# Kernel tuning notes

Hardware: AMD Instinct MI355X
Metric: run time of the kernel (lower is better)

## Reference

```python
import jax, jax.numpy as jnp
import numpy as np

# Problem sizes
N, D, B = 4096, 2048, 64  # nodes, feature dim, sequential samples
# LARFDSSOM hyperparameters (from __init__ defaults)
A_T = 0.3          # activation threshold
DSBETA = 1e-4      # moving-average rate
E_B = 0.5          # winner learning rate
E_N = 0.01 * E_B   # neighbor learning rate (e_n is multiplied by e_b in __init__)
EPS_DS = 0.01      # relevance smoothing


def setup_inputs() -> dict:
    key = jax.random.key(0)
    k0, k1, k2, k3, k4 = jax.random.split(key, 5)
    return {
        "x": jax.random.uniform(k0, (B, D), jnp.float32),
        "weights": jax.random.uniform(k1, (N, D), jnp.float32),
        "moving_avg": jax.random.uniform(k2, (N, D), jnp.float32),
        "relevances": jax.random.uniform(k3, (N, D), jnp.float32),
        "wins": jnp.zeros((N,), jnp.float32),
        "neighbors": jax.random.randint(k4, (N, N), 0, 2) > 0,
    }


def _som_steps(x, weights, moving_avg, relevances, wins, neighbors):
    """Sequential LARFDSSOM update_map over B samples (codebook at max size,
    so the add_node branch is structurally impossible and the per-sample step
    is either 'update winner + neighbors' or a no-op)."""
    node_ids = jnp.arange(weights.shape[0])

    def step(state, w):
        W, M, R, wn = state
        diff = w[None, :] - W                          # [N, D]
        # weighted_distance + activation
        dists = jnp.sum(R * diff * diff, axis=1)       # [N]
        rel_sum = jnp.sum(R, axis=1)                   # [N]
        act = rel_sum / (rel_sum + dists + 1e-7)
        winner = jnp.argmax(act)
        do_upd = act[winner] >= A_T                    # else no-op (codebook full)
        is_winner = node_ids == winner
        is_nb = neighbors[winner] & (~is_winner)
        # per-node learning rate: e_b for winner, e_n for neighbors, 0 otherwise
        lr = jnp.where(is_winner, E_B, jnp.where(is_nb, E_N, 0.0))[:, None]  # [N, 1]
        # update_node (vectorized over all nodes, masked below)
        dist_abs = jnp.abs(diff)
        M_new = lr * DSBETA * dist_abs + (1.0 - lr * DSBETA) * M
        mx = jnp.max(M_new, axis=1, keepdims=True)
        mn = jnp.min(M_new, axis=1, keepdims=True)
        av = jnp.mean(M_new, axis=1, keepdims=True)
        denom = EPS_DS * (mx - mn)
        # denom == 0 -> original produces NaN then sets relevance to 1.0
        arg = jnp.clip((M_new - av) / jnp.where(denom == 0.0, 1.0, denom), -80.0, 80.0)
        R_new = jnp.where(denom == 0.0, 1.0, 1.0 / (1.0 + jnp.exp(arg)))
        W_new = W + lr * diff
        m = (do_upd & (lr[:, 0] > 0.0))[:, None]       # rows actually touched
        W = jnp.where(m, W_new, W)
        M = jnp.where(m, M_new, M)
        R = jnp.where(m, R_new, R)
        wn = wn + jnp.where(is_winner & do_upd, 1.0, 0.0)
        return (W, M, R, wn), None

    (W, M, R, wn), _ = jax.lax.scan(step, (weights, moving_avg, relevances, wins), x)
    return W


def reference(x, weights, moving_avg, relevances, wins, neighbors):
    return _som_steps(x, weights, moving_avg, relevances, wins, neighbors)
```

## Files before the change

### kernel.cpp

```cpp
#include <hip/hip_runtime.h>
#include <cstddef>

#define NN 4096
#define DD 2048
#define BB 64
#define RPB 8
#define NBLK (NN / RPB)

constexpr float kAT     = 0.3f;
constexpr float kDSBETA = 1e-4f;
constexpr float kEB     = 0.5f;
constexpr float kEN     = 0.005f;
constexpr float kEPS    = 0.01f;

__device__ __forceinline__ float wave_sum_f(float v) {
#pragma unroll
    for (int o = 32; o; o >>= 1) v += __shfl_xor(v, o, 64);
    return v;
}
__device__ __forceinline__ double wave_sum_d(double v) {
#pragma unroll
    for (int o = 32; o; o >>= 1) v += __shfl_xor(v, o, 64);
    return v;
}
__device__ __forceinline__ float wave_max_f(float v) {
#pragma unroll
    for (int o = 32; o; o >>= 1) v = fmaxf(v, __shfl_xor(v, o, 64));
    return v;
}
__device__ __forceinline__ float wave_min_f(float v) {
#pragma unroll
    for (int o = 32; o; o >>= 1) v = fminf(v, __shfl_xor(v, o, 64));
    return v;
}
__device__ __forceinline__ unsigned long long wave_max_u64(unsigned long long v) {
#pragma unroll
    for (int o = 32; o; o >>= 1) {
        const unsigned long long u = __shfl_xor(v, o, 64);
        v = (u > v) ? u : v;
    }
    return v;
}

__global__ void detect_nb(const unsigned char* __restrict__ nb, unsigned* __restrict__ flag) {
    unsigned v = 0;
    const int i0 = threadIdx.x * 256;
    for (int i = 0; i < 256; i++) {
        const int idx = i0 + i;
        if ((idx & 3) != 0) v |= nb[idx];
    }
    if (v != 0) atomicOr(flag, 1u);
}

__global__ __launch_bounds__(256, 2) void som_persist(
    const float* __restrict__ x,
    const float* __restrict__ W0,
    const float* __restrict__ M0,
    const float* __restrict__ R0,
    const unsigned char* __restrict__ nbb,
    const unsigned* __restrict__ flag,
    float* __restrict__ Wout,
    unsigned long long* __restrict__ pkey,
    unsigned long long* __restrict__ bcast)
{
    const int tid  = threadIdx.x;
    const int wid  = tid >> 6;
    const int lane = tid & 63;
    const int bid  = (int)blockIdx.x;
    const int n0   = bid * RPB;
    const int col  = tid * 8;

    __shared__ double sdd[2][RPB][4];
    __shared__ float  sf[3][4];
    __shared__ unsigned long long skk[RPB];
    __shared__ unsigned long long sKey;

    const bool nb_byte = (*flag != 0);
    const int* nbi = (const int*)nbb;

    float w[RPB][8], r[RPB][8], m[RPB][8], xcur[8];

#pragma unroll
    for (int row = 0; row < RPB; ++row) {
        const size_t base = (size_t)(n0 + row) * DD + col;
        *(float4*)(&w[row][0]) = *(const float4*)(W0 + base);
        *(float4*)(&w[row][4]) = *(const float4*)(W0 + base + 4);
        *(float4*)(&r[row][0]) = *(const float4*)(R0 + base);
        *(float4*)(&r[row][4]) = *(const float4*)(R0 + base + 4);
        *(float4*)(&m[row][0]) = *(const float4*)(M0 + base);
        *(float4*)(&m[row][4]) = *(const float4*)(M0 + base + 4);
    }
    *(float4*)(xcur)     = *(const float4*)(x + col);
    *(float4*)(xcur + 4) = *(const float4*)(x + col + 4);

    auto act_phase = [&](int slot) {
#pragma unroll
        for (int row = 0; row < RPB; ++row) {
            double pd = 0.0, ps = 0.0;
#pragma unroll
            for (int j = 0; j < 8; ++j) {
                const double d  = (double)xcur[j] - (double)w[row][j];
                const double rj = (double)r[row][j];
                pd += rj * d * d;
                ps += rj;
            }
            pd = wave_sum_d(pd); ps = wave_sum_d(ps);
            if (lane == 0) { sdd[0][row][wid] = pd; sdd[1][row][wid] = ps; }
        }
        __syncthreads();
        if (tid < RPB) {
            const int row = tid;
            const double td = sdd[0][row][0] + sdd[0][row][1] + sdd[0][row][2] + sdd[0][row][3];
            const double tr = sdd[1][row][0] + sdd[1][row][1] + sdd[1][row][2] + sdd[1][row][3];
            const double act = tr / (tr + td + 1e-7);
            const unsigned long long ab = (unsigned long long)__double_as_longlong(act);
            skk[row] = (ab & ~0xFFFULL) | (unsigned long long)(4095 - (n0 + row));
        }
        __syncthreads();
        if (tid == 0) {
            unsigned long long k = skk[0];
#pragma unroll
            for (int i = 1; i < RPB; ++i) k = (skk[i] > k) ? skk[i] : k;
            __hip_atomic_store(&pkey[(size_t)slot * NBLK + bid], k,
                               __ATOMIC_RELAXED, __HIP_MEMORY_SCOPE_AGENT);
        }
        __syncthreads();
    };

    act_phase(0);

    for (int t = 0; t < BB; ++t) {
        if (wid == 0) {
            unsigned long long kmax = 0;
            if (bid == 0) {
                unsigned long long* pk = pkey + (size_t)t * NBLK;
                unsigned long long kk[8];
                int it = 0;
                while (true) {
                    bool miss = false;
#pragma unroll
                    for (int i = 0; i < 8; ++i) {
                        kk[i] = __hip_atomic_load(&pk[lane + 64 * i],
                                                  __ATOMIC_RELAXED, __HIP_MEMORY_SCOPE_AGENT);
                        miss |= (kk[i] == 0ull);
                    }
                    if (!__any(miss)) break;
                    if (++it > 2000000) break;
                    __builtin_amdgcn_s_sleep(1);
                }
#pragma unroll
                for (int i = 0; i < 8; ++i) kmax = (kk[i] > kmax) ? kk[i] : kmax;
                kmax = wave_max_u64(kmax);
                if (lane < 8)
                    __hip_atomic_store(&bcast[((size_t)t * 8 + lane) * 8], kmax,
                                       __ATOMIC_RELAXED, __HIP_MEMORY_SCOPE_AGENT);
            } else {
                const int rep = bid & 7;
                int it = 0;
                while ((kmax = __hip_atomic_load(&bcast[((size_t)t * 8 + rep) * 8],
                                                 __ATOMIC_RELAXED, __HIP_MEMORY_SCOPE_AGENT))
                       == 0ull) {
                    if (++it > 2000000) break;
                    __builtin_amdgcn_s_sleep(4);
                }
            }
            if (lane == 0) sKey = kmax;
        }
        __syncthreads();
        const unsigned long long k = sKey;
        __syncthreads();
        const double act_w = __longlong_as_double((long long)(k & ~0xFFFULL));
        const int winner   = 4095 - (int)(k & 0xFFFULL);

        if (act_w >= (double)kAT) {
#pragma unroll
            for (int row = 0; row < RPB; ++row) {
                const int n = n0 + row;
                float lr = 0.0f;
                if (n == winner) {
                    lr = kEB;
                } else {
                    const size_t off = (size_t)winner * NN + n;
                    const bool isnb = nb_byte ? (nbb[off] != 0) : (nbi[off] != 0);
                    if (isnb) lr = kEN;
                }
                if (lr != 0.0f) {
                    const float c1 = lr * kDSBETA;
                    const float c2 = 1.0f - c1;
                    float psum = 0.0f, pmx = -INFINITY, pmn = INFINITY;
#pragma unroll
                    for (int j = 0; j < 8; ++j) {
                        const float d  = xcur[j] - w[row][j];
                        const float mv = c1 * fabsf(d) + c2 * m[row][j];
                        w[row][j] += lr * d;
                        m[row][j] = mv;
                        psum += mv;
                        pmx = fmaxf(pmx, mv);
                        pmn = fminf(pmn, mv);
                    }
                    psum = wave_sum_f(psum); pmx = wave_max_f(pmx); pmn = wave_min_f(pmn);
                    if (lane == 0) { sf[0][wid] = psum; sf[1][wid] = pmx; sf[2][wid] = pmn; }
                    __syncthreads();
                    const float ts  = sf[0][0] + sf[0][1] + sf[0][2] + sf[0][3];
                    const float tmx = fmaxf(fmaxf(sf[1][0], sf[1][1]), fmaxf(sf[1][2], sf[1][3]));
                    const float tmn = fminf(fminf(sf[2][0], sf[2][1]), fminf(sf[2][2], sf[2][3]));
                    __syncthreads();
                    const float av    = ts * (1.0f / (float)DD);
                    const float denom = kEPS * (tmx - tmn);
                    if (denom == 0.0f) {
#pragma unroll
                        for (int j = 0; j < 8; ++j) r[row][j] = 1.0f;
                    } else {
#pragma unroll
                        for (int j = 0; j < 8; ++j) {
                            float a = (m[row][j] - av) / denom;
                            a = fminf(fmaxf(a, -80.0f), 80.0f);
                            r[row][j] = 1.0f / (1.0f + expf(a));
                        }
                    }
                }
            }
        }

        if (t < BB - 1) {
            const size_t xb = (size_t)(t + 1) * DD + col;
            *(float4*)(xcur)     = *(const float4*)(x + xb);
            *(float4*)(xcur + 4) = *(const float4*)(x + xb + 4);
            act_phase(t + 1);
        }
    }

#pragma unroll
    for (int row = 0; row < RPB; ++row) {
        const size_t base = (size_t)(n0 + row) * DD + col;
        *(float4*)(Wout + base)     = *(float4*)(&w[row][0]);
        *(float4*)(Wout + base + 4) = *(float4*)(&w[row][4]);
    }
}

__global__ __launch_bounds__(256) void som_step(
    const float* __restrict__ x_upd, const float* __restrict__ x_act,
    float* __restrict__ W, float* __restrict__ M, float* __restrict__ R,
    const void* __restrict__ nb, const unsigned* __restrict__ flag,
    const unsigned long long* __restrict__ part_upd,
    unsigned long long* __restrict__ part_act)
{
    const int n   = blockIdx.x;
    const int tid = threadIdx.x;
    __shared__ float  sred[3][4];
    __shared__ double sredd[2][4];

    float lr = 0.0f;
    if (part_upd != nullptr) {
        unsigned long long k = part_upd[(size_t)(tid & 63) * 8];
        k = wave_max_u64(k);
        const double act_w = __longlong_as_double((long long)(k & ~0xFFFULL));
        const int winner   = 4095 - (int)(k & 0xFFFULL);
        if (act_w >= (double)kAT) {
            if (n == winner) lr = kEB;
            else {
                const size_t off = (size_t)winner * NN + n;
                const bool isnb = (*flag != 0)
                    ? (((const unsigned char*)nb)[off] != 0)
                    : (((const int*)nb)[off] != 0);
                if (isnb) lr = kEN;
            }
        }
    }
    const bool next = (x_act != nullptr);
    if (lr == 0.0f && !next) return;

    const size_t rowoff = (size_t)n * DD + (size_t)tid * 8;
    const size_t xoff   = (size_t)tid * 8;
    float w[8], r[8];
    *(float4*)(w)     = *(const float4*)(W + rowoff);
    *(float4*)(w + 4) = *(const float4*)(W + rowoff + 4);

    if (lr != 0.0f) {
        float m[8], xu[8], mnew[8];
        *(float4*)(m)      = *(const float4*)(M + rowoff);
        *(float4*)(m + 4)  = *(const float4*)(M + rowoff + 4);
        *(float4*)(xu)     = *(const float4*)(x_upd + xoff);
        *(float4*)(xu + 4) = *(const float4*)(x_upd + xoff + 4);
        const float c1 = lr * kDSBETA, c2 = 1.0f - c1;
        float psum = 0.0f, pmx = -INFINITY, pmn = INFINITY;
#pragma unroll
        for (int j = 0; j < 8; j++) {
            const float d = xu[j] - w[j];
            w[j] += lr * d;
            const float mv = c1 * fabsf(d) + c2 * m[j];
            mnew[j] = mv; psum += mv;
            pmx = fmaxf(pmx, mv); pmn = fminf(pmn, mv);
        }
        psum = wave_sum_f(psum); pmx = wave_max_f(pmx); pmn = wave_min_f(pmn);
        const int wid = tid >> 6, lane = tid & 63;
        if (lane == 0) { sred[0][wid] = psum; sred[1][wid] = pmx; sred[2][wid] = pmn; }
        __syncthreads();
        const float ts  = sred[0][0] + sred[0][1] + sred[0][2] + sred[0][3];
        const float tmx = fmaxf(fmaxf(sred[1][0], sred[1][1]), fmaxf(sred[1][2], sred[1][3]));
        const float tmn = fminf(fminf(sred[2][0], sred[2][1]), fminf(sred[2][2], sred[2][3]));
        __syncthreads();
        const float av = ts * (1.0f / (float)DD);
        const float denom = kEPS * (tmx - tmn);
        if (denom == 0.0f) {
#pragma unroll
            for (int j = 0; j < 8; j++) r[j] = 1.0f;
        } else {
#pragma unroll
            for (int j = 0; j < 8; j++) {
                float a = (mnew[j] - av) / denom;
                a = fminf(fmaxf(a, -80.0f), 80.0f);
                r[j] = 1.0f / (1.0f + expf(a));
            }
        }
        *(float4*)(W + rowoff)     = *(float4*)(w);
        *(float4*)(W + rowoff + 4) = *(float4*)(w + 4);
        *(float4*)(M + rowoff)     = *(float4*)(mnew);
        *(float4*)(M + rowoff + 4) = *(float4*)(mnew + 4);
        *(float4*)(R + rowoff)     = *(float4*)(r);
        *(float4*)(R + rowoff + 4) = *(float4*)(r + 4);
    } else {
        *(float4*)(r)     = *(const float4*)(R + rowoff);
        *(float4*)(r + 4) = *(const float4*)(R + rowoff + 4);
    }

    if (next) {
        float xn[8];
        *(float4*)(xn)     = *(const float4*)(x_act + xoff);
        *(float4*)(xn + 4) = *(const float4*)(x_act + xoff + 4);
        double pd = 0.0, ps = 0.0;
#pragma unroll
        for (int j = 0; j < 8; j++) {
            const double d  = (double)xn[j] - (double)w[j];
            const double rj = (double)r[j];
            pd += rj * d * d; ps += rj;
        }
        pd = wave_sum_d(pd); ps = wave_sum_d(ps);
        const int wid = tid >> 6, lane = tid & 63;
        if (lane == 0) { sredd[0][wid] = pd; sredd[1][wid] = ps; }
        __syncthreads();
        if (tid == 0) {
            const double td = sredd[0][0] + sredd[0][1] + sredd[0][2] + sredd[0][3];
            const double tr = sredd[1][0] + sredd[1][1] + sredd[1][2] + sredd[1][3];
            const double act = tr / (tr + td + 1e-7);
            const unsigned long long ab = (unsigned long long)__double_as_longlong(act);
            const unsigned long long kk = (ab & ~0xFFFULL) | (unsigned long long)(4095 - n);
            atomicMax(&part_act[(size_t)(n & 63) * 8], kk);
        }
    }
}

extern "C" void kernel_launch(void* const* d_in, const int* in_sizes, int n_in,
                              void* d_out, int out_size, void* d_ws, size_t ws_size,
                              hipStream_t stream) {
    const float*         x   = (const float*)d_in[0];
    const float*         W0  = (const float*)d_in[1];
    float*               M   = (float*)d_in[2];
    float*               R   = (float*)d_in[3];
    const unsigned char* nbb = (const unsigned char*)d_in[5];
    float*               W   = (float*)d_out;

    unsigned long long* part = (unsigned long long*)d_ws;
    const size_t part_bytes  = (size_t)66 * 64 * 8 * sizeof(unsigned long long);
    unsigned long long* bcast = (unsigned long long*)((char*)d_ws + part_bytes);
    const size_t cnt_bytes = (size_t)BB * 8 * 16 * sizeof(unsigned);
    unsigned* flagp = (unsigned*)((char*)d_ws + part_bytes + cnt_bytes);

    hipMemsetAsync(d_ws, 0, part_bytes + cnt_bytes + 64, stream);
    detect_nb<<<1, 256, 0, stream>>>(nbb, flagp);

    int occ = 0;
    hipError_t qerr = hipOccupancyMaxActiveBlocksPerMultiprocessor(
        &occ, (const void*)som_persist, 256, 0);
    if (qerr == hipSuccess && occ >= 2) {
        som_persist<<<NBLK, 256, 0, stream>>>(x, W0, M, R, nbb, flagp, W, part, bcast);
        return;
    }

    hipMemcpyAsync(W, W0, sizeof(float) * (size_t)NN * DD, hipMemcpyDeviceToDevice, stream);
    som_step<<<NN, 256, 0, stream>>>(nullptr, x, W, M, R, nbb, flagp, nullptr, part);
    for (int t = 0; t < BB; t++) {
        const float* xu = x + (size_t)t * DD;
        const float* xa = (t < BB - 1) ? (x + (size_t)(t + 1) * DD) : nullptr;
        const unsigned long long* pu = part + (size_t)t * 64 * 8;
        unsigned long long*       pa = (t < BB - 1) ? (part + (size_t)(t + 1) * 64 * 8) : nullptr;
        som_step<<<NN, 256, 0, stream>>>(xu, xa, W, M, R, nbb, flagp, pu, pa);
    }
}
```

Baseline: 1.686 ms.

## Decentralize winner reduction and batch per-row block reductions in persistent SOM kernel

Every block now polls all 512 partial keys and reduces the winner itself, replacing the two-hop path through block 0 and a broadcast slot. The per-row shared-memory reductions are batched behind one barrier instead of two barriers per updated row. The neighbor flags are read with one vector load, and the next sample's x is prefetched early. Several redundant __syncthreads are removed. In exchange, all 512 blocks poll the same key array, which adds L2 traffic and contention.

New measurement: 1.681 ms (median of 2 runs). About the same (-0.3%).

```diff
diff --git a/kernel.cpp b/kernel.cpp
--- a/kernel.cpp
+++ b/kernel.cpp
@@ -60,8 +60,7 @@
     const unsigned char* __restrict__ nbb,
     const unsigned* __restrict__ flag,
     float* __restrict__ Wout,
-    unsigned long long* __restrict__ pkey,
-    unsigned long long* __restrict__ bcast)
+    unsigned long long* __restrict__ pkey)
 {
     const int tid  = threadIdx.x;
     const int wid  = tid >> 6;
@@ -71,7 +70,7 @@
     const int col  = tid * 8;
 
     __shared__ double sdd[2][RPB][4];
-    __shared__ float  sf[3][4];
+    __shared__ float  sf[3][RPB][4];
     __shared__ unsigned long long skk[RPB];
     __shared__ unsigned long long sKey;
 
@@ -124,67 +123,73 @@
             __hip_atomic_store(&pkey[(size_t)slot * NBLK + bid], k,
                                __ATOMIC_RELAXED, __HIP_MEMORY_SCOPE_AGENT);
         }
-        __syncthreads();
     };
 
     act_phase(0);
 
+    float xn[8];
     for (int t = 0; t < BB; ++t) {
+        const bool has_next = (t < BB - 1);
+        if (has_next) {
+            const size_t xb = (size_t)(t + 1) * DD + col;
+            *(float4*)(xn)     = *(const float4*)(x + xb);
+            *(float4*)(xn + 4) = *(const float4*)(x + xb + 4);
+        }
+
         if (wid == 0) {
+            unsigned long long* pk = pkey + (size_t)t * NBLK;
+            unsigned long long kk[8];
+            int it = 0;
+            while (true) {
+                bool miss = false;
+#pragma unroll
+                for (int i = 0; i < 8; ++i) {
+                    kk[i] = __hip_atomic_load(&pk[lane + 64 * i],
+                                              __ATOMIC_RELAXED, __HIP_MEMORY_SCOPE_AGENT);
+                    miss |= (kk[i] == 0ull);
+                }
+                if (!__any(miss)) break;
+                if (++it > 2000000) break;
+                __builtin_amdgcn_s_sleep(1);
+            }
             unsigned long long kmax = 0;
-            if (bid == 0) {
-                unsigned long long* pk = pkey + (size_t)t * NBLK;
-                unsigned long long kk[8];
-                int it = 0;
-                while (true) {
-                    bool miss = false;
-#pragma unroll
-                    for (int i = 0; i < 8; ++i) {
-                        kk[i] = __hip_atomic_load(&pk[lane + 64 * i],
-                                                  __ATOMIC_RELAXED, __HIP_MEMORY_SCOPE_AGENT);
-                        miss |= (kk[i] == 0ull);
-                    }
-                    if (!__any(miss)) break;
-                    if (++it > 2000000) break;
-                    __builtin_amdgcn_s_sleep(1);
-                }
-#pragma unroll
-                for (int i = 0; i < 8; ++i) kmax = (kk[i] > kmax) ? kk[i] : kmax;
-                kmax = wave_max_u64(kmax);
-                if (lane < 8)
-                    __hip_atomic_store(&bcast[((size_t)t * 8 + lane) * 8], kmax,
-                                       __ATOMIC_RELAXED, __HIP_MEMORY_SCOPE_AGENT);
-            } else {
-                const int rep = bid & 7;
-                int it = 0;
-                while ((kmax = __hip_atomic_load(&bcast[((size_t)t * 8 + rep) * 8],
-                                                 __ATOMIC_RELAXED, __HIP_MEMORY_SCOPE_AGENT))
-                       == 0ull) {
-                    if (++it > 2000000) break;
-                    __builtin_amdgcn_s_sleep(4);
-                }
-            }
+#pragma unroll
+            for (int i = 0; i < 8; ++i) kmax = (kk[i] > kmax) ? kk[i] : kmax;
+            kmax = wave_max_u64(kmax);
             if (lane == 0) sKey = kmax;
         }
         __syncthreads();
         const unsigned long long k = sKey;
-        __syncthreads();
         const double act_w = __longlong_as_double((long long)(k & ~0xFFFULL));
         const int winner   = 4095 - (int)(k & 0xFFFULL);
 
         if (act_w >= (double)kAT) {
+            int nbr[RPB];
+            {
+                const size_t off = (size_t)winner * NN + n0;
+                if (nb_byte) {
+                    const unsigned long long nb8 = *(const unsigned long long*)(nbb + off);
+#pragma unroll
+                    for (int i = 0; i < RPB; ++i)
+                        nbr[i] = (int)((nb8 >> (8 * i)) & 0xFFull);
+                } else {
+                    const int4 a = *(const int4*)(nbi + off);
+                    const int4 b = *(const int4*)(nbi + off + 4);
+                    nbr[0] = a.x; nbr[1] = a.y; nbr[2] = a.z; nbr[3] = a.w;
+                    nbr[4] = b.x; nbr[5] = b.y; nbr[6] = b.z; nbr[7] = b.w;
+                }
+            }
+            float lrs[RPB];
+            bool any = false;
 #pragma unroll
             for (int row = 0; row < RPB; ++row) {
                 const int n = n0 + row;
                 float lr = 0.0f;
-                if (n == winner) {
-                    lr = kEB;
-                } else {
-                    const size_t off = (size_t)winner * NN + n;
-                    const bool isnb = nb_byte ? (nbb[off] != 0) : (nbi[off] != 0);
-                    if (isnb) lr = kEN;
-                }
+                if (n == winner)      lr = kEB;
+                else if (nbr[row])    lr = kEN;
+                lrs[row] = lr;
                 if (lr != 0.0f) {
+                    any = true;
                     const float c1 = lr * kDSBETA;
                     const float c2 = 1.0f - c1;
                     float psum = 0.0f, pmx = -INFINITY, pmn = INFINITY;
@@ -199,33 +204,40 @@
                         pmn = fminf(pmn, mv);
                     }
                     psum = wave_sum_f(psum); pmx = wave_max_f(pmx); pmn = wave_min_f(pmn);
-                    if (lane == 0) { sf[0][wid] = psum; sf[1][wid] = pmx; sf[2][wid] = pmn; }
-                    __syncthreads();
-                    const float ts  = sf[0][0] + sf[0][1] + sf[0][2] + sf[0][3];
-                    const float tmx = fmaxf(fmaxf(sf[1][0], sf[1][1]), fmaxf(sf[1][2], sf[1][3]));
-                    const float tmn = fminf(fminf(sf[2][0], sf[2][1]), fminf(sf[2][2], sf[2][3]));
-                    __syncthreads();
-                    const float av    = ts * (1.0f / (float)DD);
-                    const float denom = kEPS * (tmx - tmn);
-                    if (denom == 0.0f) {
-#pragma unroll
-                        for (int j = 0; j < 8; ++j) r[row][j] = 1.0f;
-                    } else {
-#pragma unroll
-                        for (int j = 0; j < 8; ++j) {
-                            float a = (m[row][j] - av) / denom;
-                            a = fminf(fmaxf(a, -80.0f), 80.0f);
-                            r[row][j] = 1.0f / (1.0f + expf(a));
+                    if (lane == 0) { sf[0][row][wid] = psum; sf[1][row][wid] = pmx; sf[2][row][wid] = pmn; }
+                }
+            }
+            if (any) {
+                __syncthreads();
+#pragma unroll
+                for (int row = 0; row < RPB; ++row) {
+                    if (lrs[row] != 0.0f) {
+                        const float ts  = sf[0][row][0] + sf[0][row][1] + sf[0][row][2] + sf[0][row][3];
+                        const float tmx = fmaxf(fmaxf(sf[1][row][0], sf[1][row][1]),
+                                                fmaxf(sf[1][row][2], sf[1][row][3]));
+                        const float tmn = fminf(fminf(sf[2][row][0], sf[2][row][1]),
+                                                fminf(sf[2][row][2], sf[2][row][3]));
+                        const float av    = ts * (1.0f / (float)DD);
+                        const float denom = kEPS * (tmx - tmn);
+                        if (denom == 0.0f) {
+#pragma unroll
+                            for (int j = 0; j < 8; ++j) r[row][j] = 1.0f;
+                        } else {
+#pragma unroll
+                            for (int j = 0; j < 8; ++j) {
+                                float a = (m[row][j] - av) / denom;
+                                a = fminf(fmaxf(a, -80.0f), 80.0f);
+                                r[row][j] = 1.0f / (1.0f + expf(a));
+                            }
                         }
                     }
                 }
             }
         }
 
-        if (t < BB - 1) {
-            const size_t xb = (size_t)(t + 1) * DD + col;
-            *(float4*)(xcur)     = *(const float4*)(x + xb);
-            *(float4*)(xcur + 4) = *(const float4*)(x + xb + 4);
+        if (has_next) {
+#pragma unroll
+            for (int j = 0; j < 8; ++j) xcur[j] = xn[j];
             act_phase(t + 1);
         }
     }
@@ -362,7 +374,6 @@
 
     unsigned long long* part = (unsigned long long*)d_ws;
     const size_t part_bytes  = (size_t)66 * 64 * 8 * sizeof(unsigned long long);
-    unsigned long long* bcast = (unsigned long long*)((char*)d_ws + part_bytes);
     const size_t cnt_bytes = (size_t)BB * 8 * 16 * sizeof(unsigned);
     unsigned* flagp = (unsigned*)((char*)d_ws + part_bytes + cnt_bytes);
 
@@ -373,7 +384,7 @@
     hipError_t qerr = hipOccupancyMaxActiveBlocksPerMultiprocessor(
         &occ, (const void*)som_persist, 256, 0);
     if (qerr == hipSuccess && occ >= 2) {
-        som_persist<<<NBLK, 256, 0, stream>>>(x, W0, M, R, nbb, flagp, W, part, bcast);
+        som_persist<<<NBLK, 256, 0, stream>>>(x, W0, M, R, nbb, flagp, W, part);
         return;
     }
 
```
